# Performance work log

Measured on AMD Instinct MI355X. Metric: run time of the kernel, lower is better.

Reference implementation:

```python
import jax, jax.numpy as jnp
import numpy as np


def setup_inputs() -> dict:
    key = jax.random.key(0)
    ks = jax.random.split(key, 4)
    B, T, D, H, C = 256, 512, 128, 512, 128
    # xavier-uniform-like scales
    def xavier(k, shape):
        fan_in, fan_out = shape
        lim = np.sqrt(6.0 / (fan_in + fan_out))
        return jax.random.uniform(k, shape, jnp.float32, -lim, lim)
    return {
        "x": jax.random.normal(ks[0], (B, T, D), jnp.float32),
        "Whx": xavier(ks[1], (D, H)),
        "Whh": xavier(ks[2], (H, H)),
        "Wph": xavier(ks[3], (H, C)),
        "bh": jnp.zeros((H,), jnp.float32),
        "bp": jnp.zeros((C,), jnp.float32),
    }


def reference(x, Whx, Whh, Wph, bh, bp):
    B, T, D = x.shape
    H = Whh.shape[0]
    # Precompute input projections for all timesteps in one big GEMM: [B,T,H]
    xproj = jnp.einsum("btd,dh->bth", x, Whx) + bh

    def step(h, xp_t):
        h = jnp.tanh(xp_t + h @ Whh)
        return h, None

    h0 = jnp.zeros((B, H), x.dtype)
    # scan over time: xproj transposed to [T,B,H]
    h_final, _ = jax.lax.scan(step, h0, jnp.swapaxes(xproj, 0, 1))
    return h_final @ Wph + bp
```

## Files before the change

kernel.cpp:

```cpp
#include <hip/hip_runtime.h>
#include <type_traits>

typedef _Float16 f16;
typedef f16 f16x4 __attribute__((ext_vector_type(4)));
typedef f16 f16x8 __attribute__((ext_vector_type(8)));
typedef float f32x4 __attribute__((ext_vector_type(4)));
typedef unsigned int u32;

#define MFMA __builtin_amdgcn_mfma_f32_16x16x32_f16
#define WGSCOPE __HIP_MEMORY_SCOPE_WORKGROUP

constexpr int Bsz = 256, T = 512, D = 128, H = 512, C = 128;
constexpr int ROWS = 16;
constexpr int TPB  = 512;
constexpr int LDH  = H + 8;
constexpr int LDX  = D + 8;
constexpr int NTG  = H / 16;
constexpr int PKT  = 8;
constexpr int KTL  = 3;
constexpr size_t XSTRIDE = (size_t)16 * NTG * 256;

__global__ void pack_w(const float* __restrict__ W, int K, int N, int perm,
                       f16* __restrict__ out) {
    int total = K * N;
    int NT = N / 16;
    for (int idx = blockIdx.x * blockDim.x + threadIdx.x; idx < total;
         idx += gridDim.x * blockDim.x) {
        int e    = idx & 7;
        int lane = (idx >> 3) & 63;
        int tile = idx >> 9;
        int kt = tile / NT, nt = tile % NT;
        int k = kt * 32 + 8 * (lane >> 4) + e;
        int m = lane & 15;
        int n = perm ? ((nt >> 2) * 64 + (nt & 3) + 4 * m) : (nt * 16 + m);
        out[idx] = (f16)W[(size_t)k * N + n];
    }
}

__device__ __forceinline__ f16x8 load_a(const f16* base, int ld, int kt, int l15, int l4) {
    return *(const f16x8*)(base + l15 * ld + kt * 32 + 8 * l4);
}

__device__ __forceinline__ float fast_tanh(float v) {
    float e = __builtin_amdgcn_exp2f(v * 2.885390081777927f);
    return 1.f - __fdividef(2.f, e + 1.f);
}

template <typename OT>
__global__ __launch_bounds__(TPB, 2) void xproj_k(
    const float* __restrict__ x, const f16* __restrict__ wpack,
    const float* __restrict__ bh, OT* __restrict__ xp) {
    const f16* Whx_p = wpack;
    __shared__ __align__(16) f16 xb[2][ROWS][LDX];
    const int tid = threadIdx.x, lane = tid & 63, w = tid >> 6;
    const int l15 = lane & 15, l4 = lane >> 4;
    const int bt = blockIdx.x;
    const int t0 = blockIdx.y * 16;
    const int b0 = bt * ROWS;
    const int xrow = tid >> 5, xd0 = (tid & 31) * 4;
    const int ntg0 = w * 4;

    float bh4[4];
#pragma unroll
    for (int nt = 0; nt < 4; nt++) bh4[nt] = bh[w * 64 + nt + 4 * l15];
    {
        float4 v = *(const float4*)&x[((size_t)(b0 + xrow) * T + t0) * D + xd0];
        f16x4 h4 = {(f16)v.x, (f16)v.y, (f16)v.z, (f16)v.w};
        *(f16x4*)&xb[0][xrow][xd0] = h4;
    }
    __syncthreads();

    int p = 0;
    for (int tt = 0; tt < 16; tt++) {
        int t = t0 + tt;
        float4 xv;
        const bool havex = (tt + 1 < 16);
        if (havex)
            xv = *(const float4*)&x[((size_t)(b0 + xrow) * T + (t + 1)) * D + xd0];
        f32x4 acc[4];
#pragma unroll
        for (int nt = 0; nt < 4; nt++)
            acc[nt] = (f32x4){bh4[nt], bh4[nt], bh4[nt], bh4[nt]};
#pragma unroll
        for (int kt = 0; kt < D / 32; kt++) {
            f16x8 a = load_a(&xb[p][0][0], LDX, kt, l15, l4);
            const f16* btp = Whx_p + (((size_t)kt * NTG + ntg0) * 64 + lane) * 8;
#pragma unroll
            for (int nt = 0; nt < 4; nt++) {
                f16x8 b = *(const f16x8*)(btp + (size_t)nt * 512);
                acc[nt] = MFMA(a, b, acc[nt], 0, 0, 0);
            }
        }
        if (havex) {
            f16x4 h4 = {(f16)xv.x, (f16)xv.y, (f16)xv.z, (f16)xv.w};
            *(f16x4*)&xb[p ^ 1][xrow][xd0] = h4;
        }
        OT* op = xp + (((size_t)t * 16 + bt) * NTG + ntg0) * 256 + (size_t)lane * 4;
#pragma unroll
        for (int nt = 0; nt < 4; nt++) {
            if constexpr (std::is_same_v<OT, float>) {
                *(f32x4*)(op + (size_t)nt * 256) = acc[nt];
            } else {
                f16x4 v = {(f16)acc[nt][0], (f16)acc[nt][1], (f16)acc[nt][2],
                           (f16)acc[nt][3]};
                *(f16x4*)(op + (size_t)nt * 256) = v;
            }
        }
        __syncthreads();
        p ^= 1;
    }
}

template <int XP>
__global__ __launch_bounds__(TPB, 2) void rnn_main(
    const float* __restrict__ x, const f16* __restrict__ wpack,
    const void* __restrict__ xproj, const float* __restrict__ bh,
    const float* __restrict__ bp, float* __restrict__ out) {
    const f16* Whx_p = wpack;
    const f16* Whh_p = wpack + D * H;
    const f16* Wph_p = wpack + D * H + H * H;

    __shared__ __align__(16) f16 hbuf[3][ROWS][LDH];
    __shared__ __align__(16) f16 whh_lds[KTL * NTG * 64 * 8];
    __shared__ u32 pflag[8];
    __shared__ __align__(16) f16 xbuf[(XP == 0) ? 2 : 1][(XP == 0) ? ROWS : 1]
                                     [(XP == 0) ? LDX : 8];

    const int tid = threadIdx.x, lane = tid & 63, w = tid >> 6;
    const int l15 = lane & 15, l4 = lane >> 4;
    const int b0 = blockIdx.x * ROWS;
    const int xrow = tid >> 5, xd0 = (tid & 31) * 4;
    const int ntg0 = w * 4;

    f16x8 wreg[PKT][4];
#pragma unroll
    for (int kt = 0; kt < PKT; kt++)
#pragma unroll
        for (int nt = 0; nt < 4; nt++)
            wreg[kt][nt] =
                *(const f16x8*)(Whh_p + (((size_t)kt * NTG + ntg0 + nt) * 64 + lane) * 8);

    {
        const f16* src = Whh_p + (size_t)PKT * NTG * 512;
        for (int i = tid; i < KTL * NTG * 64; i += TPB)
            *(f16x8*)&whh_lds[(size_t)i * 8] = *(const f16x8*)(src + (size_t)i * 8);
    }
    for (int i = tid; i < ROWS * LDH; i += TPB) (&hbuf[0][0][0])[i] = (f16)0.f;
    if (tid < 8) pflag[tid] = 0u;

    float bh4[4];
    const float* xpf = nullptr;
    const f16* xph = nullptr;
    if constexpr (XP == 1) {
        xpf = (const float*)xproj + (((size_t)blockIdx.x * NTG + ntg0) * 64 + lane) * 4;
    } else if constexpr (XP == 2) {
        xph = (const f16*)xproj + (((size_t)blockIdx.x * NTG + ntg0) * 64 + lane) * 4;
    } else {
#pragma unroll
        for (int nt = 0; nt < 4; nt++) bh4[nt] = bh[w * 64 + nt + 4 * l15];
        float4 v = *(const float4*)&x[((size_t)(b0 + xrow) * T + 0) * D + xd0];
        f16x4 h4 = {(f16)v.x, (f16)v.y, (f16)v.z, (f16)v.w};
        *(f16x4*)&xbuf[0][xrow][xd0] = h4;
    }

    f16x8 sA[4], sB[4];
    {
        const f16* wb0 = Whh_p + ((size_t)ntg0 * 64 + lane) * 8;
#pragma unroll
        for (int nt = 0; nt < 4; nt++)
            sA[nt] = *(const f16x8*)(wb0 + ((size_t)11 * NTG + nt) * 512);
#pragma unroll
        for (int nt = 0; nt < 4; nt++)
            sB[nt] = *(const f16x8*)(wb0 + ((size_t)12 * NTG + nt) * 512);
    }
    __syncthreads();
    __builtin_amdgcn_s_setprio(1);

    auto spin = [&](int v, u32 tgt) {
        if constexpr (XP != 0) {
            if (v != w) {
                if (__hip_atomic_load(&pflag[v], __ATOMIC_ACQUIRE, WGSCOPE) >= tgt)
                    return;
                __builtin_amdgcn_s_setprio(0);
                do {
                    __builtin_amdgcn_s_sleep(1);
                } while (__hip_atomic_load(&pflag[v], __ATOMIC_ACQUIRE, WGSCOPE) < tgt);
                __builtin_amdgcn_s_setprio(1);
            }
        }
    };

    auto body = [&](u32 t, const f16* hb, f16* hw, f16x8(&bA)[4], f16x8(&bB)[4],
                    int pp) {
        uintptr_t whu = (uintptr_t)Whh_p;
        asm volatile("" : "+s"(whu));
        const f16* wbase = (const f16*)whu + ((size_t)ntg0 * 64 + lane) * 8;
        u32 zo = 0;
        asm volatile("" : "+v"(zo));
        const f16x8* wlds = (const f16x8*)whh_lds + zo;

        f32x4 xr32[4];
        f16x4 xr16[4];
        if constexpr (XP == 1) {
            const float* xq = xpf + (size_t)t * XSTRIDE;
#pragma unroll
            for (int nt = 0; nt < 4; nt++) xr32[nt] = *(const f32x4*)(xq + (size_t)nt * 256);
        } else if constexpr (XP == 2) {
            const f16* xq = xph + (size_t)t * XSTRIDE;
#pragma unroll
            for (int nt = 0; nt < 4; nt++) xr16[nt] = *(const f16x4*)(xq + (size_t)nt * 256);
        }

        f32x4 acc[4];
        if constexpr (XP == 0) {
#pragma unroll
            for (int nt = 0; nt < 4; nt++)
                acc[nt] = (f32x4){bh4[nt], bh4[nt], bh4[nt], bh4[nt]};
        } else {
#pragma unroll
            for (int nt = 0; nt < 4; nt++) acc[nt] = (f32x4){0.f, 0.f, 0.f, 0.f};
        }

        if constexpr (XP == 0) {
            float4 xv;
            const bool havex = (t + 1 < T);
            if (havex)
                xv = *(const float4*)&x[((size_t)(b0 + xrow) * T + (t + 1)) * D + xd0];
            uintptr_t wxu = (uintptr_t)Whx_p;
            asm volatile("" : "+s"(wxu));
            const f16* wxs = (const f16*)wxu;
#pragma unroll
            for (int kt = 0; kt < D / 32; kt++) {
                f16x8 a = load_a(&xbuf[pp][0][0], LDX, kt, l15, l4);
                const f16* bt = wxs + (((size_t)kt * NTG + ntg0) * 64 + lane) * 8;
#pragma unroll
                for (int nt = 0; nt < 4; nt++) {
                    f16x8 b = *(const f16x8*)(bt + (size_t)nt * 512);
                    acc[nt] = MFMA(a, b, acc[nt], 0, 0, 0);
                }
            }
            if (havex) {
                f16x4 h4 = {(f16)xv.x, (f16)xv.y, (f16)xv.z, (f16)xv.w};
                *(f16x4*)&xbuf[pp ^ 1][xrow][xd0] = h4;
            }
        }

        auto LS = [&](int kt, f16x8(&bf)[4]) {
#pragma unroll
            for (int nt = 0; nt < 4; nt++)
                bf[nt] = *(const f16x8*)(wbase + ((size_t)kt * NTG + nt) * 512);
        };
        auto PK = [&](int kt) {
            f16x8 a = load_a(hb, LDH, kt, l15, l4);
#pragma unroll
            for (int nt = 0; nt < 4; nt++)
                acc[nt] = MFMA(a, wreg[kt][nt], acc[nt], 0, 0, 0);
        };
        auto CL = [&](int ktl) {
            f16x8 a = load_a(hb, LDH, PKT + ktl, l15, l4);
#pragma unroll
            for (int nt = 0; nt < 4; nt++)
                acc[nt] = MFMA(a, wlds[((size_t)ktl * NTG + ntg0 + nt) * 64 + lane],
                               acc[nt], 0, 0, 0);
        };
        auto CS = [&](int kt, f16x8(&bf)[4]) {
            f16x8 a = load_a(hb, LDH, kt, l15, l4);
#pragma unroll
            for (int nt = 0; nt < 4; nt++) acc[nt] = MFMA(a, bf[nt], acc[nt], 0, 0, 0);
        };

         spin(0, t); PK(0);
                     PK(1);
         spin(5, t); CS(11, bA); LS(13, bA);
         spin(1, t); PK(2);
                     PK(3);
         spin(6, t); CS(12, bB); LS(14, bB);
         spin(4, t); CL(0);
         spin(2, t); PK(4);
                     CS(13, bA); LS(15, bA);
                     PK(5);
                     CL(1);
         spin(7, t); CS(14, bB); LS(11, bB);
         spin(3, t); PK(6);
                     CL(2);
                     CS(15, bA); LS(12, bA);
                     PK(7);

#pragma unroll
        for (int r = 0; r < 4; r++) {
            f16x4 hv;
#pragma unroll
            for (int nt = 0; nt < 4; nt++) {
                float v = acc[nt][r];
                if constexpr (XP == 1) v += xr32[nt][r];
                else if constexpr (XP == 2) v += (float)xr16[nt][r];
                hv[nt] = (f16)fast_tanh(v);
            }
            *(f16x4*)&hw[(l4 * 4 + r) * LDH + w * 64 + 4 * l15] = hv;
        }
        if constexpr (XP != 0) {
            if (lane == 0)
                __hip_atomic_store(&pflag[w], t + 1, __ATOMIC_RELEASE, WGSCOPE);
        } else {
            __syncthreads();
        }
    };

    f16* r0 = &hbuf[0][0][0];
    f16* r1 = &hbuf[1][0][0];
    f16* r2 = &hbuf[2][0][0];
    for (u32 t = 0; t < T; t += 2) {
        body(t,     r0, r1, sA, sB, 0);
        body(t + 1, r1, r2, sB, sA, 1);
        f16* n0 = r2; f16* n1 = r0; f16* n2 = r1;
        r0 = n0; r1 = n1; r2 = n2;
    }

    if constexpr (XP != 0) {
        __builtin_amdgcn_s_setprio(0);
        for (;;) {
            u32 f = __hip_atomic_load(&pflag[lane & 7], __ATOMIC_ACQUIRE, WGSCOPE);
            if (((u32)__ballot(f >= (u32)T) & 0xffu) == 0xffu) break;
            __builtin_amdgcn_s_sleep(1);
        }
        __builtin_amdgcn_s_setprio(1);
    } else {
        __syncthreads();
    }
    {
        float bpv = bp[w * 16 + l15];
        f32x4 acc = {bpv, bpv, bpv, bpv};
#pragma unroll 4
        for (int kt = 0; kt < H / 32; kt++) {
            f16x8 a = load_a(r0, LDH, kt, l15, l4);
            f16x8 b = *(const f16x8*)(Wph_p + (((size_t)kt * (C / 16) + w) * 64 + lane) * 8);
            acc = MFMA(a, b, acc, 0, 0, 0);
        }
#pragma unroll
        for (int r = 0; r < 4; r++)
            out[(size_t)(b0 + l4 * 4 + r) * C + w * 16 + l15] = acc[r];
    }
}

extern "C" void kernel_launch(void* const* d_in, const int* in_sizes, int n_in,
                              void* d_out, int out_size, void* d_ws, size_t ws_size,
                              hipStream_t stream) {
    const float* x   = (const float*)d_in[0];
    const float* Whx = (const float*)d_in[1];
    const float* Whh = (const float*)d_in[2];
    const float* Wph = (const float*)d_in[3];
    const float* bh  = (const float*)d_in[4];
    const float* bp  = (const float*)d_in[5];

    f16* wp = (f16*)d_ws;
    pack_w<<<dim3(128), 256, 0, stream>>>(Whx, D, H, 1, wp);
    pack_w<<<dim3(512), 256, 0, stream>>>(Whh, H, H, 1, wp + D * H);
    pack_w<<<dim3(128), 256, 0, stream>>>(Wph, H, C, 0, wp + D * H + H * H);

    const size_t wbytes = (size_t)(D * H + H * H + H * C) * sizeof(f16);
    const size_t xpel   = (size_t)T * 16 * NTG * 256;

    if (ws_size >= wbytes + xpel * sizeof(float)) {
        float* xpb = (float*)((char*)d_ws + wbytes);
        xproj_k<float><<<dim3(16, T / 16), TPB, 0, stream>>>(x, wp, bh, xpb);
        rnn_main<1><<<dim3(Bsz / ROWS), TPB, 0, stream>>>(x, wp, xpb, bh, bp,
                                                          (float*)d_out);
    } else if (ws_size >= wbytes + xpel * sizeof(f16)) {
        f16* xpb = (f16*)((char*)d_ws + wbytes);
        xproj_k<f16><<<dim3(16, T / 16), TPB, 0, stream>>>(x, wp, bh, xpb);
        rnn_main<2><<<dim3(Bsz / ROWS), TPB, 0, stream>>>(x, wp, xpb, bh, bp,
                                                          (float*)d_out);
    } else {
        rnn_main<0><<<dim3(Bsz / ROWS), TPB, 0, stream>>>(x, wp, nullptr, bh, bp,
                                                          (float*)d_out);
    }
}
```

Measured before the change: 1.322 ms.

## Stagger odd-wave k-order schedule and shrink h buffer to double buffering

Odd waves now run a different k-tile order: they start with the LDS-resident and register-staged slices and wait on the other producer waves in a different sequence. Their staged Whh slices are preloaded accordingly. The aim is to spread out the cross-wave flag waits so the eight waves do not all stall on the same producer. The hidden-state ring drops from three buffers to two, which cuts LDS use and relies on the flag waits to prevent write-after-read hazards. The loop is split into two instantiations selected by wave parity, which adds code size and uses `#pragma unroll 1`.

```diff
diff --git a/kernel.cpp b/kernel.cpp
--- a/kernel.cpp
+++ b/kernel.cpp
@@ -120,7 +120,7 @@
     const f16* Whh_p = wpack + D * H;
     const f16* Wph_p = wpack + D * H + H * H;
 
-    __shared__ __align__(16) f16 hbuf[3][ROWS][LDH];
+    __shared__ __align__(16) f16 hbuf[2][ROWS][LDH];
     __shared__ __align__(16) f16 whh_lds[KTL * NTG * 64 * 8];
     __shared__ u32 pflag[8];
     __shared__ __align__(16) f16 xbuf[(XP == 0) ? 2 : 1][(XP == 0) ? ROWS : 1]
@@ -165,13 +165,15 @@
 
     f16x8 sA[4], sB[4];
     {
+        const int k1 = (w & 1) ? 13 : 11;
+        const int k2 = (w & 1) ? 14 : 12;
         const f16* wb0 = Whh_p + ((size_t)ntg0 * 64 + lane) * 8;
 #pragma unroll
         for (int nt = 0; nt < 4; nt++)
-            sA[nt] = *(const f16x8*)(wb0 + ((size_t)11 * NTG + nt) * 512);
+            sA[nt] = *(const f16x8*)(wb0 + ((size_t)k1 * NTG + nt) * 512);
 #pragma unroll
         for (int nt = 0; nt < 4; nt++)
-            sB[nt] = *(const f16x8*)(wb0 + ((size_t)12 * NTG + nt) * 512);
+            sB[nt] = *(const f16x8*)(wb0 + ((size_t)k2 * NTG + nt) * 512);
     }
     __syncthreads();
     __builtin_amdgcn_s_setprio(1);
@@ -191,7 +193,8 @@
     };
 
     auto body = [&](u32 t, const f16* hb, f16* hw, f16x8(&bA)[4], f16x8(&bB)[4],
-                    int pp) {
+                    int pp, auto oddc) {
+        constexpr bool ODD = decltype(oddc)::value;
         uintptr_t whu = (uintptr_t)Whh_p;
         asm volatile("" : "+s"(whu));
         const f16* wbase = (const f16*)whu + ((size_t)ntg0 * 64 + lane) * 8;
@@ -269,22 +272,41 @@
             for (int nt = 0; nt < 4; nt++) acc[nt] = MFMA(a, bf[nt], acc[nt], 0, 0, 0);
         };
 
-         spin(0, t); PK(0);
-                     PK(1);
-         spin(5, t); CS(11, bA); LS(13, bA);
-         spin(1, t); PK(2);
-                     PK(3);
-         spin(6, t); CS(12, bB); LS(14, bB);
-         spin(4, t); CL(0);
-         spin(2, t); PK(4);
-                     CS(13, bA); LS(15, bA);
-                     PK(5);
-                     CL(1);
-         spin(7, t); CS(14, bB); LS(11, bB);
-         spin(3, t); PK(6);
-                     CL(2);
-                     CS(15, bA); LS(12, bA);
-                     PK(7);
+        if constexpr (!ODD) {
+            spin(0, t); PK(0);
+                        PK(1);
+            spin(5, t); CS(11, bA); LS(13, bA);
+            spin(1, t); PK(2);
+                        PK(3);
+            spin(6, t); CS(12, bB); LS(14, bB);
+            spin(4, t); CL(0);
+            spin(2, t); PK(4);
+                        CS(13, bA); LS(15, bA);
+                        PK(5);
+                        CL(1);
+            spin(7, t); CS(14, bB); LS(11, bB);
+            spin(3, t); PK(6);
+                        CL(2);
+                        CS(15, bA); LS(12, bA);
+                        PK(7);
+        } else {
+            spin(6, t); CS(13, bA); LS(15, bA);
+            spin(4, t); CL(0);
+            spin(7, t); CS(14, bB); LS(11, bB);
+                        CL(1);
+            spin(5, t); CL(2);
+                        CS(15, bA); LS(12, bA);
+                        CS(11, bB); LS(13, bB);
+            spin(0, t); PK(0);
+                        CS(12, bA); LS(14, bA);
+                        PK(1);
+            spin(1, t); PK(2);
+                        PK(3);
+            spin(2, t); PK(4);
+                        PK(5);
+            spin(3, t); PK(6);
+                        PK(7);
+        }
 
 #pragma unroll
         for (int r = 0; r < 4; r++) {
@@ -306,15 +328,17 @@
         }
     };
 
-    f16* r0 = &hbuf[0][0][0];
-    f16* r1 = &hbuf[1][0][0];
-    f16* r2 = &hbuf[2][0][0];
-    for (u32 t = 0; t < T; t += 2) {
-        body(t,     r0, r1, sA, sB, 0);
-        body(t + 1, r1, r2, sB, sA, 1);
-        f16* n0 = r2; f16* n1 = r0; f16* n2 = r1;
-        r0 = n0; r1 = n1; r2 = n2;
-    }
+    f16* const h0 = &hbuf[0][0][0];
+    f16* const h1 = &hbuf[1][0][0];
+    auto mainloop = [&](auto oddc) {
+#pragma unroll 1
+        for (u32 t = 0; t < T; t += 2) {
+            body(t,     h0, h1, sA, sB, 0, oddc);
+            body(t + 1, h1, h0, sB, sA, 1, oddc);
+        }
+    };
+    if ((w & 1) == 0) mainloop(std::integral_constant<bool, false>{});
+    else              mainloop(std::integral_constant<bool, true>{});
 
     if constexpr (XP != 0) {
         __builtin_amdgcn_s_setprio(0);
@@ -332,7 +356,7 @@
         f32x4 acc = {bpv, bpv, bpv, bpv};
 #pragma unroll 4
         for (int kt = 0; kt < H / 32; kt++) {
-            f16x8 a = load_a(r0, LDH, kt, l15, l4);
+            f16x8 a = load_a(h0, LDH, kt, l15, l4);
             f16x8 b = *(const f16x8*)(Wph_p + (((size_t)kt * (C / 16) + w) * 64 + lane) * 8);
             acc = MFMA(a, b, acc, 0, 0, 0);
         }
```

After: 1.379 ms. +4.3%, slower.
